# Kernel tuning notes

Measured on AMD Instinct MI355X. Metric: run time of the kernel, lower is better.

Reference implementation:

```python
import jax, jax.numpy as jnp
import numpy as np

D_MODEL = 1024
NUM_HEADS = 4
EXPAND_K = 1.0
EXPAND_V = 2.0
KEY_DIM = int(D_MODEL * EXPAND_K)      # 1024
VALUE_DIM = int(D_MODEL * EXPAND_V)    # 2048
HEAD_K = KEY_DIM // NUM_HEADS          # 256
HEAD_V = VALUE_DIM // NUM_HEADS        # 512
CHUNK = 64
EPS = 1e-5
ROPE_BASE = 10000.0


def setup_inputs() -> dict:
    key = jax.random.key(0)
    ks = jax.random.split(key, 7)
    B, T = 4, 2048
    s = 0.02
    return {
        "x": jax.random.normal(ks[0], (B, T, D_MODEL), dtype=jnp.float32),
        "Wq": jax.random.normal(ks[1], (KEY_DIM, D_MODEL), dtype=jnp.float32) * s,
        "Wk": jax.random.normal(ks[2], (KEY_DIM, D_MODEL), dtype=jnp.float32) * s,
        "Wv": jax.random.normal(ks[3], (VALUE_DIM, D_MODEL), dtype=jnp.float32) * s,
        "Wg": jax.random.normal(ks[4], (VALUE_DIM, D_MODEL), dtype=jnp.float32) * s,
        "Wo": jax.random.normal(ks[5], (D_MODEL, VALUE_DIM), dtype=jnp.float32) * s,
        "gnorm_w": jnp.ones((HEAD_V,), dtype=jnp.float32),
    }


def _apply_rotary(q, k):
    # q,k: [B,T,H,dk]; NeoX-style (non-interleaved) rotary on full head dim
    d = q.shape[-1]
    half = d // 2
    inv_freq = 1.0 / (ROPE_BASE ** (jnp.arange(0, d, 2, dtype=jnp.float32) / d))
    t = jnp.arange(q.shape[1], dtype=jnp.float32)
    freqs = t[:, None] * inv_freq[None, :]          # [T, d/2]
    cos = jnp.cos(freqs)[None, :, None, :]
    sin = jnp.sin(freqs)[None, :, None, :]

    def rot(x):
        x1, x2 = x[..., :half], x[..., half:]
        return jnp.concatenate([x1 * cos - x2 * sin, x2 * cos + x1 * sin], axis=-1)

    return rot(q), rot(k)


def _chunk_retention(q, k, v, gamma):
    # q,k: [B,T,H,dk]; v: [B,T,H,dv]; gamma: [H] per-head decay
    B, T, H, dk = q.shape
    dv = v.shape[-1]
    C = CHUNK
    N = T // C
    qc = q.reshape(B, N, C, H, dk).transpose(1, 0, 3, 2, 4)  # [N,B,H,C,dk]
    kc = k.reshape(B, N, C, H, dk).transpose(1, 0, 3, 2, 4)
    vc = v.reshape(B, N, C, H, dv).transpose(1, 0, 3, 2, 4)  # [N,B,H,C,dv]

    i = jnp.arange(C, dtype=jnp.float32)
    cross_dec = gamma[:, None] ** (i + 1.0)          # [H,C] gamma^{i+1}: query decay vs incoming state
    k_dec = gamma[:, None] ** (C - 1.0 - i)          # [H,C] key decay toward chunk end
    diff = i[:, None] - i[None, :]                   # [C,C]
    mask = jnp.where(diff >= 0, gamma[:, None, None] ** diff, 0.0)  # [H,C,C]
    gC = gamma ** C                                  # [H]

    def step(S, inp):
        # S: [B,H,dk,dv]
        qb, kb, vb = inp
        attn = jnp.einsum('bhid,bhjd->bhij', qb, kb) * mask
        o_intra = jnp.einsum('bhij,bhjv->bhiv', attn, vb)
        o_inter = jnp.einsum('bhid,bhdv->bhiv', qb * cross_dec[:, :, None], S)
        S_new = gC[:, None, None] * S + jnp.einsum('bhjd,bhjv->bhdv', kb * k_dec[:, :, None], vb)
        return S_new, o_intra + o_inter

    S0 = jnp.zeros((B, H, dk, dv), dtype=q.dtype)
    _, o = jax.lax.scan(step, S0, (qc, kc, vc))      # o: [N,B,H,C,dv]
    return o.transpose(1, 0, 3, 2, 4).reshape(B, T, H, dv)


def reference(x, Wq, Wk, Wv, Wg, Wo, gnorm_w):
    B, T, _ = x.shape
    H = NUM_HEADS
    q = (x @ Wq.T).reshape(B, T, H, HEAD_K)
    k = (x @ Wk.T).reshape(B, T, H, HEAD_K)
    v = (x @ Wv.T).reshape(B, T, H, HEAD_V)
    g = (x @ Wg.T).reshape(B, T, H, HEAD_V)

    q, k = _apply_rotary(q, k)
    q = q * (HEAD_K ** -0.5)

    # fixed multi-scale decays: gamma_h = 1 - 2^{-5-h}
    gamma = 1.0 - jnp.exp2(-5.0 - jnp.arange(H, dtype=jnp.float32))

    o = _chunk_retention(q, k, v, gamma)             # [B,T,H,dv]

    # per-head RMSNorm + swish gate, then output projection
    var = jnp.mean(o * o, axis=-1, keepdims=True)
    o = o * jax.lax.rsqrt(var + EPS) * gnorm_w
    o = o * (g * jax.nn.sigmoid(g))
    return o.reshape(B, T, H * HEAD_V) @ Wo.T
```

## Files before the change

kernel.cpp:

```cpp
#include <hip/hip_runtime.h>
#include <cstdint>
#include <cstddef>

#define T_SEQ 2048
#define DM    1024
#define HK    256
#define HV    512
#define NH    4
#define KDIM  1024
#define VDIM  2048

typedef __attribute__((ext_vector_type(8))) short bf16x8;
typedef __attribute__((ext_vector_type(4))) float f32x4;
#define AS1 __attribute__((address_space(1)))
#define AS3 __attribute__((address_space(3)))

static __device__ inline unsigned short f2bf(float f) {
  unsigned u = __float_as_uint(f);
  unsigned rnd = 0x7fffu + ((u >> 16) & 1u);
  return (unsigned short)((u + rnd) >> 16);
}
static __device__ inline float bf2f(unsigned short h) {
  unsigned u = ((unsigned)h) << 16;
  return __uint_as_float(u);
}

__global__ __launch_bounds__(256) void cast_all(const float* __restrict__ x,
                                                const float* __restrict__ Wq,
                                                const float* __restrict__ Wk,
                                                const float* __restrict__ Wv,
                                                const float* __restrict__ Wg,
                                                const float* __restrict__ Wo,
                                                unsigned short* __restrict__ xh,  unsigned short* __restrict__ xl,
                                                unsigned short* __restrict__ wqh, unsigned short* __restrict__ wql,
                                                unsigned short* __restrict__ wkh, unsigned short* __restrict__ wkl,
                                                unsigned short* __restrict__ wvh, unsigned short* __restrict__ wvl,
                                                unsigned short* __restrict__ wgh, unsigned short* __restrict__ wgl,
                                                unsigned short* __restrict__ woh, unsigned short* __restrict__ wol) {
  const int bx = blockIdx.x;
  const float* in; unsigned short* hi; unsigned short* lo; int rel;
  if (bx < 8192)       { in = x;  hi = xh;  lo = xl;  rel = bx; }
  else if (bx < 9216)  { in = Wq; hi = wqh; lo = wql; rel = bx - 8192; }
  else if (bx < 10240) { in = Wk; hi = wkh; lo = wkl; rel = bx - 9216; }
  else if (bx < 12288) { in = Wv; hi = wvh; lo = wvl; rel = bx - 10240; }
  else if (bx < 14336) { in = Wg; hi = wgh; lo = wgl; rel = bx - 12288; }
  else                 { in = Wo; hi = woh; lo = wol; rel = bx - 14336; }
  int i = rel * 256 + threadIdx.x;
  float4 v = ((const float4*)in)[i];
  ushort4 h, l;
  h.x = f2bf(v.x); l.x = f2bf(v.x - bf2f(h.x));
  h.y = f2bf(v.y); l.y = f2bf(v.y - bf2f(h.y));
  h.z = f2bf(v.z); l.z = f2bf(v.z - bf2f(h.z));
  h.w = f2bf(v.w); l.w = f2bf(v.w - bf2f(h.w));
  ((ushort4*)hi)[i] = h;
  ((ushort4*)lo)[i] = l;
}

__global__ __launch_bounds__(256) void gemm_bf16s(const unsigned short* __restrict__ Ah,
                                                  const unsigned short* __restrict__ Al,
                                                  const unsigned short* __restrict__ Wh,
                                                  const unsigned short* __restrict__ Wl,
                                                  float* __restrict__ C,
                                                  int M, int N, int K) {
  __shared__ unsigned short AhS[128 * 32];
  __shared__ unsigned short AlS[128 * 32];
  __shared__ unsigned short WhS[128 * 32];
  __shared__ unsigned short WlS[128 * 32];
  const int t = threadIdx.x;
  const int l = t & 63;
  const int w = t >> 6;
  const int bm = blockIdx.y * 128;
  const int bn = blockIdx.x * 128;
  const int wm = (w >> 1) * 64;
  const int wn = (w & 1) * 64;

  f32x4 acc[4][4];
#pragma unroll
  for (int i = 0; i < 4; ++i)
#pragma unroll
    for (int j = 0; j < 4; ++j)
#pragma unroll
      for (int r = 0; r < 4; ++r) acc[i][j][r] = 0.f;

  const int srow = w * 32 + (l >> 2);
  const int scol = (l & 3) * 8;
  const size_t gOffA = (size_t)(bm + srow) * K + scol;
  const size_t gOffW = (size_t)(bn + srow) * K + scol;
  const size_t rowStep = (size_t)16 * K;
  unsigned short* lAh0 = &AhS[(w * 32) * 32];
  unsigned short* lAh1 = &AhS[(w * 32 + 16) * 32];
  unsigned short* lAl0 = &AlS[(w * 32) * 32];
  unsigned short* lAl1 = &AlS[(w * 32 + 16) * 32];
  unsigned short* lWh0 = &WhS[(w * 32) * 32];
  unsigned short* lWh1 = &WhS[(w * 32 + 16) * 32];
  unsigned short* lWl0 = &WlS[(w * 32) * 32];
  unsigned short* lWl1 = &WlS[(w * 32 + 16) * 32];

  for (int k0 = 0; k0 < K; k0 += 32) {
    __syncthreads();
    __builtin_amdgcn_global_load_lds((const AS1 void*)(Ah + gOffA + k0),           (AS3 void*)lAh0, 16, 0, 0);
    __builtin_amdgcn_global_load_lds((const AS1 void*)(Ah + gOffA + rowStep + k0), (AS3 void*)lAh1, 16, 0, 0);
    __builtin_amdgcn_global_load_lds((const AS1 void*)(Al + gOffA + k0),           (AS3 void*)lAl0, 16, 0, 0);
    __builtin_amdgcn_global_load_lds((const AS1 void*)(Al + gOffA + rowStep + k0), (AS3 void*)lAl1, 16, 0, 0);
    __builtin_amdgcn_global_load_lds((const AS1 void*)(Wh + gOffW + k0),           (AS3 void*)lWh0, 16, 0, 0);
    __builtin_amdgcn_global_load_lds((const AS1 void*)(Wh + gOffW + rowStep + k0), (AS3 void*)lWh1, 16, 0, 0);
    __builtin_amdgcn_global_load_lds((const AS1 void*)(Wl + gOffW + k0),           (AS3 void*)lWl0, 16, 0, 0);
    __builtin_amdgcn_global_load_lds((const AS1 void*)(Wl + gOffW + rowStep + k0), (AS3 void*)lWl1, 16, 0, 0);
    __syncthreads();

    bf16x8 ah[4], al[4], bh[4], bl[4];
#pragma unroll
    for (int i = 0; i < 4; ++i) {
      int aoff = (wm + i * 16 + (l & 15)) * 32 + (l >> 4) * 8;
      int boff = (wn + i * 16 + (l & 15)) * 32 + (l >> 4) * 8;
      ah[i] = *(const bf16x8*)&AhS[aoff];
      al[i] = *(const bf16x8*)&AlS[aoff];
      bh[i] = *(const bf16x8*)&WhS[boff];
      bl[i] = *(const bf16x8*)&WlS[boff];
    }
#pragma unroll
    for (int i = 0; i < 4; ++i)
#pragma unroll
      for (int j = 0; j < 4; ++j) {
        acc[i][j] = __builtin_amdgcn_mfma_f32_16x16x32_bf16(ah[i], bh[j], acc[i][j], 0, 0, 0);
        acc[i][j] = __builtin_amdgcn_mfma_f32_16x16x32_bf16(ah[i], bl[j], acc[i][j], 0, 0, 0);
        acc[i][j] = __builtin_amdgcn_mfma_f32_16x16x32_bf16(al[i], bh[j], acc[i][j], 0, 0, 0);
      }
  }

  const int cr = (l >> 4) * 4;
  const int cc = l & 15;
#pragma unroll
  for (int i = 0; i < 4; ++i)
#pragma unroll
    for (int j = 0; j < 4; ++j)
#pragma unroll
      for (int r = 0; r < 4; ++r)
        C[(size_t)(bm + wm + i * 16 + cr + r) * N + (bn + wn + j * 16 + cc)] = acc[i][j][r];
}

__global__ __launch_bounds__(256) void gemm_qkv(const unsigned short* __restrict__ Ah,
                                                const unsigned short* __restrict__ Al,
                                                const unsigned short* __restrict__ wqh,
                                                const unsigned short* __restrict__ wql,
                                                const unsigned short* __restrict__ wkh,
                                                const unsigned short* __restrict__ wkl,
                                                const unsigned short* __restrict__ wvh,
                                                const unsigned short* __restrict__ wvl,
                                                float* __restrict__ q,
                                                float* __restrict__ kk,
                                                float* __restrict__ v) {
  const int K = 1024;
  const int bx = blockIdx.x;
  const unsigned short* Wh; const unsigned short* Wl; float* C; int N; int bn;
  if (bx < 8)       { Wh = wqh; Wl = wql; C = q;  N = 1024; bn = bx * 128; }
  else if (bx < 16) { Wh = wkh; Wl = wkl; C = kk; N = 1024; bn = (bx - 8) * 128; }
  else              { Wh = wvh; Wl = wvl; C = v;  N = 2048; bn = (bx - 16) * 128; }

  __shared__ unsigned short AhS[128 * 32];
  __shared__ unsigned short AlS[128 * 32];
  __shared__ unsigned short WhS[128 * 32];
  __shared__ unsigned short WlS[128 * 32];
  const int t = threadIdx.x;
  const int l = t & 63;
  const int w = t >> 6;
  const int bm = blockIdx.y * 128;
  const int wm = (w >> 1) * 64;
  const int wn = (w & 1) * 64;

  f32x4 acc[4][4];
#pragma unroll
  for (int i = 0; i < 4; ++i)
#pragma unroll
    for (int j = 0; j < 4; ++j)
#pragma unroll
      for (int r = 0; r < 4; ++r) acc[i][j][r] = 0.f;

  const int srow = w * 32 + (l >> 2);
  const int scol = (l & 3) * 8;
  const size_t gOffA = (size_t)(bm + srow) * K + scol;
  const size_t gOffW = (size_t)(bn + srow) * K + scol;
  const size_t rowStep = (size_t)16 * K;
  unsigned short* lAh0 = &AhS[(w * 32) * 32];
  unsigned short* lAh1 = &AhS[(w * 32 + 16) * 32];
  unsigned short* lAl0 = &AlS[(w * 32) * 32];
  unsigned short* lAl1 = &AlS[(w * 32 + 16) * 32];
  unsigned short* lWh0 = &WhS[(w * 32) * 32];
  unsigned short* lWh1 = &WhS[(w * 32 + 16) * 32];
  unsigned short* lWl0 = &WlS[(w * 32) * 32];
  unsigned short* lWl1 = &WlS[(w * 32 + 16) * 32];

  for (int k0 = 0; k0 < K; k0 += 32) {
    __syncthreads();
    __builtin_amdgcn_global_load_lds((const AS1 void*)(Ah + gOffA + k0),           (AS3 void*)lAh0, 16, 0, 0);
    __builtin_amdgcn_global_load_lds((const AS1 void*)(Ah + gOffA + rowStep + k0), (AS3 void*)lAh1, 16, 0, 0);
    __builtin_amdgcn_global_load_lds((const AS1 void*)(Al + gOffA + k0),           (AS3 void*)lAl0, 16, 0, 0);
    __builtin_amdgcn_global_load_lds((const AS1 void*)(Al + gOffA + rowStep + k0), (AS3 void*)lAl1, 16, 0, 0);
    __builtin_amdgcn_global_load_lds((const AS1 void*)(Wh + gOffW + k0),           (AS3 void*)lWh0, 16, 0, 0);
    __builtin_amdgcn_global_load_lds((const AS1 void*)(Wh + gOffW + rowStep + k0), (AS3 void*)lWh1, 16, 0, 0);
    __builtin_amdgcn_global_load_lds((const AS1 void*)(Wl + gOffW + k0),           (AS3 void*)lWl0, 16, 0, 0);
    __builtin_amdgcn_global_load_lds((const AS1 void*)(Wl + gOffW + rowStep + k0), (AS3 void*)lWl1, 16, 0, 0);
    __syncthreads();

    bf16x8 ah[4], al[4], bh[4], bl[4];
#pragma unroll
    for (int i = 0; i < 4; ++i) {
      int aoff = (wm + i * 16 + (l & 15)) * 32 + (l >> 4) * 8;
      int boff = (wn + i * 16 + (l & 15)) * 32 + (l >> 4) * 8;
      ah[i] = *(const bf16x8*)&AhS[aoff];
      al[i] = *(const bf16x8*)&AlS[aoff];
      bh[i] = *(const bf16x8*)&WhS[boff];
      bl[i] = *(const bf16x8*)&WlS[boff];
    }
#pragma unroll
    for (int i = 0; i < 4; ++i)
#pragma unroll
      for (int j = 0; j < 4; ++j) {
        acc[i][j] = __builtin_amdgcn_mfma_f32_16x16x32_bf16(ah[i], bh[j], acc[i][j], 0, 0, 0);
        acc[i][j] = __builtin_amdgcn_mfma_f32_16x16x32_bf16(ah[i], bl[j], acc[i][j], 0, 0, 0);
        acc[i][j] = __builtin_amdgcn_mfma_f32_16x16x32_bf16(al[i], bh[j], acc[i][j], 0, 0, 0);
      }
  }

  const int cr = (l >> 4) * 4;
  const int cc = l & 15;
#pragma unroll
  for (int i = 0; i < 4; ++i)
#pragma unroll
    for (int j = 0; j < 4; ++j)
#pragma unroll
      for (int r = 0; r < 4; ++r)
        C[(size_t)(bm + wm + i * 16 + cr + r) * N + (bn + wn + j * 16 + cc)] = acc[i][j][r];
}

__global__ __launch_bounds__(256) void rope_kernel(float* __restrict__ q,
                                                   float* __restrict__ k) {
  int idx = blockIdx.x * 256 + threadIdx.x;
  int f  = idx & 127;
  int h  = (idx >> 7) & 3;
  int tt = (idx >> 9) & 2047;
  int b  = idx >> 20;
  size_t a0 = ((size_t)(b * T_SEQ + tt)) * KDIM + h * HK + f;
  size_t a1 = a0 + 128;
  float invf = powf(10000.0f, -(float)f * (1.0f / 128.0f));
  float ang  = (float)tt * invf;
  float s, c;
  sincosf(ang, &s, &c);
  float q1 = q[a0], q2 = q[a1];
  q[a0] = (q1 * c - q2 * s) * 0.0625f;
  q[a1] = (q2 * c + q1 * s) * 0.0625f;
  float k1 = k[a0], k2 = k[a1];
  k[a0] = k1 * c - k2 * s;
  k[a1] = k2 * c + k1 * s;
}

__global__ __launch_bounds__(256) void retn_intra(const float* __restrict__ q,
                                                  const float* __restrict__ k,
                                                  const float* __restrict__ v,
                                                  float* __restrict__ o) {
  const int n = blockIdx.x, h = blockIdx.y, b = blockIdx.z;
  const int t = threadIdx.x;
  const int t0 = n * 64;
  __shared__ float gpow[65];
  __shared__ __align__(16) float qS[64][68];
  __shared__ __align__(16) float kS[64][68];
  __shared__ __align__(16) float attnS[64][68];
  if (t <= 64) {
    float gamma = 1.0f - exp2f(-5.0f - (float)h);
    gpow[t] = powf(gamma, (float)t);
  }
  const size_t baseQK = (size_t)(b * T_SEQ + t0) * KDIM + h * HK;
  const size_t baseV  = (size_t)(b * T_SEQ + t0) * VDIM + h * HV;
  const int i0 = (t >> 4) * 4;
  const int j0 = (t & 15) * 4;
  float acc[4][4] = {};
  for (int s = 0; s < 4; ++s) {
    __syncthreads();
    __builtin_amdgcn_sched_barrier(0);
#pragma unroll
    for (int r = 0; r < 4; ++r) {
      int idx = t + 256 * r;
      int row = idx >> 4, c4 = (idx & 15) * 4;
      *(float4*)&qS[row][c4] = *(const float4*)&q[baseQK + (size_t)row * KDIM + s * 64 + c4];
      *(float4*)&kS[row][c4] = *(const float4*)&k[baseQK + (size_t)row * KDIM + s * 64 + c4];
    }
    __syncthreads();
    __builtin_amdgcn_sched_barrier(0);
    for (int d = 0; d < 64; d += 4) {
      float4 a0 = *(const float4*)&qS[i0 + 0][d];
      float4 a1 = *(const float4*)&qS[i0 + 1][d];
      float4 a2 = *(const float4*)&qS[i0 + 2][d];
      float4 a3 = *(const float4*)&qS[i0 + 3][d];
      float4 b0 = *(const float4*)&kS[j0 + 0][d];
      float4 b1 = *(const float4*)&kS[j0 + 1][d];
      float4 b2 = *(const float4*)&kS[j0 + 2][d];
      float4 b3 = *(const float4*)&kS[j0 + 3][d];
      acc[0][0]=fmaf(a0.x,b0.x,acc[0][0]); acc[0][0]=fmaf(a0.y,b0.y,acc[0][0]); acc[0][0]=fmaf(a0.z,b0.z,acc[0][0]); acc[0][0]=fmaf(a0.w,b0.w,acc[0][0]);
      acc[0][1]=fmaf(a0.x,b1.x,acc[0][1]); acc[0][1]=fmaf(a0.y,b1.y,acc[0][1]); acc[0][1]=fmaf(a0.z,b1.z,acc[0][1]); acc[0][1]=fmaf(a0.w,b1.w,acc[0][1]);
      acc[0][2]=fmaf(a0.x,b2.x,acc[0][2]); acc[0][2]=fmaf(a0.y,b2.y,acc[0][2]); acc[0][2]=fmaf(a0.z,b2.z,acc[0][2]); acc[0][2]=fmaf(a0.w,b2.w,acc[0][2]);
      acc[0][3]=fmaf(a0.x,b3.x,acc[0][3]); acc[0][3]=fmaf(a0.y,b3.y,acc[0][3]); acc[0][3]=fmaf(a0.z,b3.z,acc[0][3]); acc[0][3]=fmaf(a0.w,b3.w,acc[0][3]);
      acc[1][0]=fmaf(a1.x,b0.x,acc[1][0]); acc[1][0]=fmaf(a1.y,b0.y,acc[1][0]); acc[1][0]=fmaf(a1.z,b0.z,acc[1][0]); acc[1][0]=fmaf(a1.w,b0.w,acc[1][0]);
      acc[1][1]=fmaf(a1.x,b1.x,acc[1][1]); acc[1][1]=fmaf(a1.y,b1.y,acc[1][1]); acc[1][1]=fmaf(a1.z,b1.z,acc[1][1]); acc[1][1]=fmaf(a1.w,b1.w,acc[1][1]);
      acc[1][2]=fmaf(a1.x,b2.x,acc[1][2]); acc[1][2]=fmaf(a1.y,b2.y,acc[1][2]); acc[1][2]=fmaf(a1.z,b2.z,acc[1][2]); acc[1][2]=fmaf(a1.w,b2.w,acc[1][2]);
      acc[1][3]=fmaf(a1.x,b3.x,acc[1][3]); acc[1][3]=fmaf(a1.y,b3.y,acc[1][3]); acc[1][3]=fmaf(a1.z,b3.z,acc[1][3]); acc[1][3]=fmaf(a1.w,b3.w,acc[1][3]);
      acc[2][0]=fmaf(a2.x,b0.x,acc[2][0]); acc[2][0]=fmaf(a2.y,b0.y,acc[2][0]); acc[2][0]=fmaf(a2.z,b0.z,acc[2][0]); acc[2][0]=fmaf(a2.w,b0.w,acc[2][0]);
      acc[2][1]=fmaf(a2.x,b1.x,acc[2][1]); acc[2][1]=fmaf(a2.y,b1.y,acc[2][1]); acc[2][1]=fmaf(a2.z,b1.z,acc[2][1]); acc[2][1]=fmaf(a2.w,b1.w,acc[2][1]);
      acc[2][2]=fmaf(a2.x,b2.x,acc[2][2]); acc[2][2]=fmaf(a2.y,b2.y,acc[2][2]); acc[2][2]=fmaf(a2.z,b2.z,acc[2][2]); acc[2][2]=fmaf(a2.w,b2.w,acc[2][2]);
      acc[2][3]=fmaf(a2.x,b3.x,acc[2][3]); acc[2][3]=fmaf(a2.y,b3.y,acc[2][3]); acc[2][3]=fmaf(a2.z,b3.z,acc[2][3]); acc[2][3]=fmaf(a2.w,b3.w,acc[2][3]);
      acc[3][0]=fmaf(a3.x,b0.x,acc[3][0]); acc[3][0]=fmaf(a3.y,b0.y,acc[3][0]); acc[3][0]=fmaf(a3.z,b0.z,acc[3][0]); acc[3][0]=fmaf(a3.w,b0.w,acc[3][0]);
      acc[3][1]=fmaf(a3.x,b1.x,acc[3][1]); acc[3][1]=fmaf(a3.y,b1.y,acc[3][1]); acc[3][1]=fmaf(a3.z,b1.z,acc[3][1]); acc[3][1]=fmaf(a3.w,b1.w,acc[3][1]);
      acc[3][2]=fmaf(a3.x,b2.x,acc[3][2]); acc[3][2]=fmaf(a3.y,b2.y,acc[3][2]); acc[3][2]=fmaf(a3.z,b2.z,acc[3][2]); acc[3][2]=fmaf(a3.w,b2.w,acc[3][2]);
      acc[3][3]=fmaf(a3.x,b3.x,acc[3][3]); acc[3][3]=fmaf(a3.y,b3.y,acc[3][3]); acc[3][3]=fmaf(a3.z,b3.z,acc[3][3]); acc[3][3]=fmaf(a3.w,b3.w,acc[3][3]);
    }
  }
  __syncthreads();
#pragma unroll
  for (int ii = 0; ii < 4; ++ii)
#pragma unroll
    for (int jj = 0; jj < 4; ++jj) {
      int i = i0 + ii, j = j0 + jj;
      attnS[i][j] = (i >= j) ? acc[ii][jj] * gpow[i - j] : 0.0f;
    }
  float (*vS)[68] = qS;
  for (int vb = 0; vb < 8; ++vb) {
    __syncthreads();
    __builtin_amdgcn_sched_barrier(0);
#pragma unroll
    for (int r = 0; r < 4; ++r) {
      int idx = t + 256 * r;
      int row = idx >> 4, c4 = (idx & 15) * 4;
      *(float4*)&vS[row][c4] = *(const float4*)&v[baseV + (size_t)row * VDIM + vb * 64 + c4];
    }
    __syncthreads();
    __builtin_amdgcn_sched_barrier(0);
    float oa[4][4] = {};
    for (int j = 0; j < 64; j += 4) {
      float4 p0 = *(const float4*)&attnS[i0 + 0][j];
      float4 p1 = *(const float4*)&attnS[i0 + 1][j];
      float4 p2 = *(const float4*)&attnS[i0 + 2][j];
      float4 p3 = *(const float4*)&attnS[i0 + 3][j];
      float4 v0 = *(const float4*)&vS[j + 0][j0];
      float4 v1 = *(const float4*)&vS[j + 1][j0];
      float4 v2 = *(const float4*)&vS[j + 2][j0];
      float4 v3 = *(const float4*)&vS[j + 3][j0];
      oa[0][0]=fmaf(p0.x,v0.x,oa[0][0]); oa[0][0]=fmaf(p0.y,v1.x,oa[0][0]); oa[0][0]=fmaf(p0.z,v2.x,oa[0][0]); oa[0][0]=fmaf(p0.w,v3.x,oa[0][0]);
      oa[0][1]=fmaf(p0.x,v0.y,oa[0][1]); oa[0][1]=fmaf(p0.y,v1.y,oa[0][1]); oa[0][1]=fmaf(p0.z,v2.y,oa[0][1]); oa[0][1]=fmaf(p0.w,v3.y,oa[0][1]);
      oa[0][2]=fmaf(p0.x,v0.z,oa[0][2]); oa[0][2]=fmaf(p0.y,v1.z,oa[0][2]); oa[0][2]=fmaf(p0.z,v2.z,oa[0][2]); oa[0][2]=fmaf(p0.w,v3.z,oa[0][2]);
      oa[0][3]=fmaf(p0.x,v0.w,oa[0][3]); oa[0][3]=fmaf(p0.y,v1.w,oa[0][3]); oa[0][3]=fmaf(p0.z,v2.w,oa[0][3]); oa[0][3]=fmaf(p0.w,v3.w,oa[0][3]);
      oa[1][0]=fmaf(p1.x,v0.x,oa[1][0]); oa[1][0]=fmaf(p1.y,v1.x,oa[1][0]); oa[1][0]=fmaf(p1.z,v2.x,oa[1][0]); oa[1][0]=fmaf(p1.w,v3.x,oa[1][0]);
      oa[1][1]=fmaf(p1.x,v0.y,oa[1][1]); oa[1][1]=fmaf(p1.y,v1.y,oa[1][1]); oa[1][1]=fmaf(p1.z,v2.y,oa[1][1]); oa[1][1]=fmaf(p1.w,v3.y,oa[1][1]);
      oa[1][2]=fmaf(p1.x,v0.z,oa[1][2]); oa[1][2]=fmaf(p1.y,v1.z,oa[1][2]); oa[1][2]=fmaf(p1.z,v2.z,oa[1][2]); oa[1][2]=fmaf(p1.w,v3.z,oa[1][2]);
      oa[1][3]=fmaf(p1.x,v0.w,oa[1][3]); oa[1][3]=fmaf(p1.y,v1.w,oa[1][3]); oa[1][3]=fmaf(p1.z,v2.w,oa[1][3]); oa[1][3]=fmaf(p1.w,v3.w,oa[1][3]);
      oa[2][0]=fmaf(p2.x,v0.x,oa[2][0]); oa[2][0]=fmaf(p2.y,v1.x,oa[2][0]); oa[2][0]=fmaf(p2.z,v2.x,oa[2][0]); oa[2][0]=fmaf(p2.w,v3.x,oa[2][0]);
      oa[2][1]=fmaf(p2.x,v0.y,oa[2][1]); oa[2][1]=fmaf(p2.y,v1.y,oa[2][1]); oa[2][1]=fmaf(p2.z,v2.y,oa[2][1]); oa[2][1]=fmaf(p2.w,v3.y,oa[2][1]);
      oa[2][2]=fmaf(p2.x,v0.z,oa[2][2]); oa[2][2]=fmaf(p2.y,v1.z,oa[2][2]); oa[2][2]=fmaf(p2.z,v2.z,oa[2][2]); oa[2][2]=fmaf(p2.w,v3.z,oa[2][2]);
      oa[2][3]=fmaf(p2.x,v0.w,oa[2][3]); oa[2][3]=fmaf(p2.y,v1.w,oa[2][3]); oa[2][3]=fmaf(p2.z,v2.w,oa[2][3]); oa[2][3]=fmaf(p2.w,v3.w,oa[2][3]);
      oa[3][0]=fmaf(p3.x,v0.x,oa[3][0]); oa[3][0]=fmaf(p3.y,v1.x,oa[3][0]); oa[3][0]=fmaf(p3.z,v2.x,oa[3][0]); oa[3][0]=fmaf(p3.w,v3.x,oa[3][0]);
      oa[3][1]=fmaf(p3.x,v0.y,oa[3][1]); oa[3][1]=fmaf(p3.y,v1.y,oa[3][1]); oa[3][1]=fmaf(p3.z,v2.y,oa[3][1]); oa[3][1]=fmaf(p3.w,v3.y,oa[3][1]);
      oa[3][2]=fmaf(p3.x,v0.z,oa[3][2]); oa[3][2]=fmaf(p3.y,v1.z,oa[3][2]); oa[3][2]=fmaf(p3.z,v2.z,oa[3][2]); oa[3][2]=fmaf(p3.w,v3.z,oa[3][2]);
      oa[3][3]=fmaf(p3.x,v0.w,oa[3][3]); oa[3][3]=fmaf(p3.y,v1.w,oa[3][3]); oa[3][3]=fmaf(p3.z,v2.w,oa[3][3]); oa[3][3]=fmaf(p3.w,v3.w,oa[3][3]);
    }
#pragma unroll
    for (int ii = 0; ii < 4; ++ii)
      *(float4*)&o[baseV + (size_t)(i0 + ii) * VDIM + vb * 64 + j0] =
          make_float4(oa[ii][0], oa[ii][1], oa[ii][2], oa[ii][3]);
  }
}


__global__ __launch_bounds__(256) void retn_gstate(const float* __restrict__ k,
                                                   const float* __restrict__ v,
                                                   float* __restrict__ Tbuf) {
  const int bh = blockIdx.x; const int b = bh >> 2, h = bh & 3;
  const int g = blockIdx.y;
  const int dkt = blockIdx.z >> 2, dvt = blockIdx.z & 3;
  const int t = threadIdx.x;
  __shared__ float gpow[65];
  __shared__ __align__(16) float kS[64][132];
  __shared__ __align__(16) float vS[64][132];
  if (t <= 64) gpow[t] = powf(1.0f - exp2f(-5.0f - (float)h), (float)t);
  __syncthreads();
  const float gC = gpow[64];
  const size_t baseK = (size_t)(b * T_SEQ + g * 512) * KDIM + h * HK + dkt * 128;
  const size_t baseV = (size_t)(b * T_SEQ + g * 512) * VDIM + h * HV + dvt * 128;
  const int dk0 = (t & 15) * 4;
  const int c0  = (t >> 4) * 4;
  float S[2][2][4][4] = {};
  for (int c = 0; c < 8; ++c) {
    const int t0 = c * 64;
    __syncthreads();
    __builtin_amdgcn_sched_barrier(0);
#pragma unroll
    for (int r = 0; r < 8; ++r) {
      int idx = t + 256 * r; int row = idx >> 5, c4 = (idx & 31) * 4;
      float4 kv = *(const float4*)&k[baseK + (size_t)(t0 + row) * KDIM + c4];
      float kd = gpow[63 - row];
      kv.x *= kd; kv.y *= kd; kv.z *= kd; kv.w *= kd;
      *(float4*)&kS[row][c4] = kv;
      *(float4*)&vS[row][c4] = *(const float4*)&v[baseV + (size_t)(t0 + row) * VDIM + c4];
    }
    __syncthreads();
    __builtin_amdgcn_sched_barrier(0);
#pragma unroll
    for (int p = 0; p < 2; ++p)
#pragma unroll
      for (int qh = 0; qh < 2; ++qh)
#pragma unroll
        for (int ii = 0; ii < 4; ++ii)
#pragma unroll
          for (int jj = 0; jj < 4; ++jj) S[p][qh][ii][jj] *= gC;
    for (int j = 0; j < 64; ++j) {
      float4 ka = *(const float4*)&kS[j][dk0];
      float4 kb = *(const float4*)&kS[j][dk0 + 64];
      float4 va = *(const float4*)&vS[j][c0];
      float4 vb = *(const float4*)&vS[j][c0 + 64];
      float kr[8] = {ka.x, ka.y, ka.z, ka.w, kb.x, kb.y, kb.z, kb.w};
      float vr[8] = {va.x, va.y, va.z, va.w, vb.x, vb.y, vb.z, vb.w};
#pragma unroll
      for (int ii = 0; ii < 8; ++ii)
#pragma unroll
        for (int jj = 0; jj < 8; ++jj)
          S[ii >> 2][jj >> 2][ii & 3][jj & 3] =
              fmaf(kr[ii], vr[jj], S[ii >> 2][jj >> 2][ii & 3][jj & 3]);
    }
  }
  const size_t tbRow = ((size_t)g * 16 + bh) * 256 + dkt * 128 + dk0;
  const size_t tbCol = (size_t)dvt * 128 + c0;
#pragma unroll
  for (int p = 0; p < 2; ++p)
#pragma unroll
    for (int ii = 0; ii < 4; ++ii) {
      size_t rowb = (tbRow + p * 64 + ii) * 512 + tbCol;
      *(float4*)&Tbuf[rowb]      = make_float4(S[p][0][ii][0], S[p][0][ii][1], S[p][0][ii][2], S[p][0][ii][3]);
      *(float4*)&Tbuf[rowb + 64] = make_float4(S[p][1][ii][0], S[p][1][ii][1], S[p][1][ii][2], S[p][1][ii][3]);
    }
}

__global__ __launch_bounds__(256) void retn_scan(float* __restrict__ Tbuf) {
  int i = blockIdx.x * 256 + threadIdx.x;
  int h = (i >> 15) & 3;
  float gamma = 1.0f - exp2f(-5.0f - (float)h);
  float gG = powf(gamma, 512.0f);
  float4* T = (float4*)Tbuf;
  const int slab = 524288;
  float4 t0 = T[i], t1 = T[i + slab], t2 = T[i + 2 * slab];
  float4 s2, s3;
  s2.x = fmaf(gG, t0.x, t1.x); s2.y = fmaf(gG, t0.y, t1.y);
  s2.z = fmaf(gG, t0.z, t1.z); s2.w = fmaf(gG, t0.w, t1.w);
  s3.x = fmaf(gG, s2.x, t2.x); s3.y = fmaf(gG, s2.y, t2.y);
  s3.z = fmaf(gG, s2.z, t2.z); s3.w = fmaf(gG, s2.w, t2.w);
  T[i + slab] = s2; T[i + 2 * slab] = s3;
}

__global__ __launch_bounds__(256) void retn_inter2(const float* __restrict__ q,
                                                   const float* __restrict__ k,
                                                   const float* __restrict__ v,
                                                   float* __restrict__ o,
                                                   const float* __restrict__ Sbuf) {
  const int bh = blockIdx.x; const int b = bh >> 2, h = bh & 3;
  const int g = blockIdx.y;
  const int dvt = blockIdx.z;
  const int t = threadIdx.x;
  __shared__ float gpow[65];
  __shared__ __align__(16) float qS[64][68];
  __shared__ __align__(16) float kS[64][68];
  __shared__ __align__(16) float sS[64][68];
  __shared__ __align__(16) float vS[64][68];
  if (t <= 64) gpow[t] = powf(1.0f - exp2f(-5.0f - (float)h), (float)t);
  __syncthreads();
  const float gC = gpow[64];
  const int rq = (t & 15) * 4;
  const int c0 = (t >> 4) * 4;
  const int i0 = (t >> 4) * 4;
  const int v0 = (t & 15) * 4;
  const size_t baseQK = (size_t)(b * T_SEQ + g * 512) * KDIM + h * HK;
  const size_t baseV  = (size_t)(b * T_SEQ + g * 512) * VDIM + h * HV + (size_t)dvt * 64;

  float S[4][4][4];
  if (g > 0) {
    const size_t sb = (((size_t)(g - 1) * 16 + bh) * 256) * 512 + (size_t)dvt * 64 + c0;
#pragma unroll
    for (int b4 = 0; b4 < 4; ++b4)
#pragma unroll
      for (int i = 0; i < 4; ++i) {
        float4 tmp = *(const float4*)&Sbuf[sb + (size_t)(b4 * 64 + rq + i) * 512];
        S[b4][i][0] = tmp.x; S[b4][i][1] = tmp.y; S[b4][i][2] = tmp.z; S[b4][i][3] = tmp.w;
      }
  } else {
#pragma unroll
    for (int b4 = 0; b4 < 4; ++b4)
#pragma unroll
      for (int i = 0; i < 4; ++i) {
        S[b4][i][0] = 0.f; S[b4][i][1] = 0.f; S[b4][i][2] = 0.f; S[b4][i][3] = 0.f;
      }
  }

  for (int c = 0; c < 8; ++c) {
    const int t0 = c * 64;
    const bool doO = (g > 0 || c > 0);
    __syncthreads();
    __builtin_amdgcn_sched_barrier(0);
#pragma unroll
    for (int r = 0; r < 4; ++r) {
      int idx = t + 256 * r; int row = idx >> 4, c4 = (idx & 15) * 4;
      *(float4*)&vS[row][c4] = *(const float4*)&v[baseV + (size_t)(t0 + row) * VDIM + c4];
    }
    float oa[4][4] = {};
#pragma unroll
    for (int b4 = 0; b4 < 4; ++b4) {
      __syncthreads();
      __builtin_amdgcn_sched_barrier(0);
      if (doO) {
#pragma unroll
        for (int i = 0; i < 4; ++i)
          *(float4*)&sS[rq + i][c0] =
              make_float4(S[b4][i][0], S[b4][i][1], S[b4][i][2], S[b4][i][3]);
#pragma unroll
        for (int r = 0; r < 4; ++r) {
          int idx = t + 256 * r; int row = idx >> 4, c4 = (idx & 15) * 4;
          float4 qv = *(const float4*)&q[baseQK + (size_t)(t0 + row) * KDIM + b4 * 64 + c4];
          float gp = gpow[row + 1];
          qv.x *= gp; qv.y *= gp; qv.z *= gp; qv.w *= gp;
          *(float4*)&qS[row][c4] = qv;
        }
      }
#pragma unroll
      for (int r = 0; r < 4; ++r) {
        int idx = t + 256 * r; int row = idx >> 4, c4 = (idx & 15) * 4;
        float4 kv = *(const float4*)&k[baseQK + (size_t)(t0 + row) * KDIM + b4 * 64 + c4];
        float kd = gpow[63 - row];
        kv.x *= kd; kv.y *= kd; kv.z *= kd; kv.w *= kd;
        *(float4*)&kS[row][c4] = kv;
      }
      __syncthreads();
      __builtin_amdgcn_sched_barrier(0);
      if (doO) {
        for (int d = 0; d < 64; d += 4) {
          float4 a0 = *(const float4*)&qS[i0 + 0][d];
          float4 a1 = *(const float4*)&qS[i0 + 1][d];
          float4 a2 = *(const float4*)&qS[i0 + 2][d];
          float4 a3 = *(const float4*)&qS[i0 + 3][d];
          float4 s0 = *(const float4*)&sS[d + 0][v0];
          float4 s1 = *(const float4*)&sS[d + 1][v0];
          float4 s2 = *(const float4*)&sS[d + 2][v0];
          float4 s3 = *(const float4*)&sS[d + 3][v0];
          oa[0][0]=fmaf(a0.x,s0.x,oa[0][0]); oa[0][0]=fmaf(a0.y,s1.x,oa[0][0]); oa[0][0]=fmaf(a0.z,s2.x,oa[0][0]); oa[0][0]=fmaf(a0.w,s3.x,oa[0][0]);
          oa[0][1]=fmaf(a0.x,s0.y,oa[0][1]); oa[0][1]=fmaf(a0.y,s1.y,oa[0][1]); oa[0][1]=fmaf(a0.z,s2.y,oa[0][1]); oa[0][1]=fmaf(a0.w,s3.y,oa[0][1]);
          oa[0][2]=fmaf(a0.x,s0.z,oa[0][2]); oa[0][2]=fmaf(a0.y,s1.z,oa[0][2]); oa[0][2]=fmaf(a0.z,s2.z,oa[0][2]); oa[0][2]=fmaf(a0.w,s3.z,oa[0][2]);
          oa[0][3]=fmaf(a0.x,s0.w,oa[0][3]); oa[0][3]=fmaf(a0.y,s1.w,oa[0][3]); oa[0][3]=fmaf(a0.z,s2.w,oa[0][3]); oa[0][3]=fmaf(a0.w,s3.w,oa[0][3]);
          oa[1][0]=fmaf(a1.x,s0.x,oa[1][0]); oa[1][0]=fmaf(a1.y,s1.x,oa[1][0]); oa[1][0]=fmaf(a1.z,s2.x,oa[1][0]); oa[1][0]=fmaf(a1.w,s3.x,oa[1][0]);
          oa[1][1]=fmaf(a1.x,s0.y,oa[1][1]); oa[1][1]=fmaf(a1.y,s1.y,oa[1][1]); oa[1][1]=fmaf(a1.z,s2.y,oa[1][1]); oa[1][1]=fmaf(a1.w,s3.y,oa[1][1]);
          oa[1][2]=fmaf(a1.x,s0.z,oa[1][2]); oa[1][2]=fmaf(a1.y,s1.z,oa[1][2]); oa[1][2]=fmaf(a1.z,s2.z,oa[1][2]); oa[1][2]=fmaf(a1.w,s3.z,oa[1][2]);
          oa[1][3]=fmaf(a1.x,s0.w,oa[1][3]); oa[1][3]=fmaf(a1.y,s1.w,oa[1][3]); oa[1][3]=fmaf(a1.z,s2.w,oa[1][3]); oa[1][3]=fmaf(a1.w,s3.w,oa[1][3]);
          oa[2][0]=fmaf(a2.x,s0.x,oa[2][0]); oa[2][0]=fmaf(a2.y,s1.x,oa[2][0]); oa[2][0]=fmaf(a2.z,s2.x,oa[2][0]); oa[2][0]=fmaf(a2.w,s3.x,oa[2][0]);
          oa[2][1]=fmaf(a2.x,s0.y,oa[2][1]); oa[2][1]=fmaf(a2.y,s1.y,oa[2][1]); oa[2][1]=fmaf(a2.z,s2.y,oa[2][1]); oa[2][1]=fmaf(a2.w,s3.y,oa[2][1]);
          oa[2][2]=fmaf(a2.x,s0.z,oa[2][2]); oa[2][2]=fmaf(a2.y,s1.z,oa[2][2]); oa[2][2]=fmaf(a2.z,s2.z,oa[2][2]); oa[2][2]=fmaf(a2.w,s3.z,oa[2][2]);
          oa[2][3]=fmaf(a2.x,s0.w,oa[2][3]); oa[2][3]=fmaf(a2.y,s1.w,oa[2][3]); oa[2][3]=fmaf(a2.z,s2.w,oa[2][3]); oa[2][3]=fmaf(a2.w,s3.w,oa[2][3]);
          oa[3][0]=fmaf(a3.x,s0.x,oa[3][0]); oa[3][0]=fmaf(a3.y,s1.x,oa[3][0]); oa[3][0]=fmaf(a3.z,s2.x,oa[3][0]); oa[3][0]=fmaf(a3.w,s3.x,oa[3][0]);
          oa[3][1]=fmaf(a3.x,s0.y,oa[3][1]); oa[3][1]=fmaf(a3.y,s1.y,oa[3][1]); oa[3][1]=fmaf(a3.z,s2.y,oa[3][1]); oa[3][1]=fmaf(a3.w,s3.y,oa[3][1]);
          oa[3][2]=fmaf(a3.x,s0.z,oa[3][2]); oa[3][2]=fmaf(a3.y,s1.z,oa[3][2]); oa[3][2]=fmaf(a3.z,s2.z,oa[3][2]); oa[3][2]=fmaf(a3.w,s3.z,oa[3][2]);
          oa[3][3]=fmaf(a3.x,s0.w,oa[3][3]); oa[3][3]=fmaf(a3.y,s1.w,oa[3][3]); oa[3][3]=fmaf(a3.z,s2.w,oa[3][3]); oa[3][3]=fmaf(a3.w,s3.w,oa[3][3]);
        }
      }
#pragma unroll
      for (int ii = 0; ii < 4; ++ii) {
        S[b4][ii][0] *= gC; S[b4][ii][1] *= gC; S[b4][ii][2] *= gC; S[b4][ii][3] *= gC;
      }
      for (int j = 0; j < 64; ++j) {
        float4 kv = *(const float4*)&kS[j][rq];
        float4 vv = *(const float4*)&vS[j][c0];
        S[b4][0][0] = fmaf(kv.x, vv.x, S[b4][0][0]); S[b4][0][1] = fmaf(kv.x, vv.y, S[b4][0][1]);
        S[b4][0][2] = fmaf(kv.x, vv.z, S[b4][0][2]); S[b4][0][3] = fmaf(kv.x, vv.w, S[b4][0][3]);
        S[b4][1][0] = fmaf(kv.y, vv.x, S[b4][1][0]); S[b4][1][1] = fmaf(kv.y, vv.y, S[b4][1][1]);
        S[b4][1][2] = fmaf(kv.y, vv.z, S[b4][1][2]); S[b4][1][3] = fmaf(kv.y, vv.w, S[b4][1][3]);
        S[b4][2][0] = fmaf(kv.z, vv.x, S[b4][2][0]); S[b4][2][1] = fmaf(kv.z, vv.y, S[b4][2][1]);
        S[b4][2][2] = fmaf(kv.z, vv.z, S[b4][2][2]); S[b4][2][3] = fmaf(kv.z, vv.w, S[b4][2][3]);
        S[b4][3][0] = fmaf(kv.w, vv.x, S[b4][3][0]); S[b4][3][1] = fmaf(kv.w, vv.y, S[b4][3][1]);
        S[b4][3][2] = fmaf(kv.w, vv.z, S[b4][3][2]); S[b4][3][3] = fmaf(kv.w, vv.w, S[b4][3][3]);
      }
    }
    if (doO) {
#pragma unroll
      for (int ii = 0; ii < 4; ++ii) {
        size_t addr = baseV + (size_t)(t0 + i0 + ii) * VDIM + v0;
        float4 ov = *(const float4*)&o[addr];
        ov.x += oa[ii][0]; ov.y += oa[ii][1]; ov.z += oa[ii][2]; ov.w += oa[ii][3];
        *(float4*)&o[addr] = ov;
      }
    }
  }
}

__global__ __launch_bounds__(256) void norm_gate_cast(const float* __restrict__ o,
                                                      const float* __restrict__ g,
                                                      const float* __restrict__ gnw,
                                                      unsigned short* __restrict__ oh,
                                                      unsigned short* __restrict__ ol) {
  const int row = blockIdx.x;
  const size_t base = (size_t)row * 512;
  const int t = threadIdx.x;
  float x0 = o[base + t], x1 = o[base + t + 256];
  float ss = x0 * x0 + x1 * x1;
#pragma unroll
  for (int off = 32; off > 0; off >>= 1) ss += __shfl_down(ss, off, 64);
  __shared__ float wsum[4];
  if ((t & 63) == 0) wsum[t >> 6] = ss;
  __syncthreads();
  float tot = wsum[0] + wsum[1] + wsum[2] + wsum[3];
  float scale = rsqrtf(tot * (1.0f / 512.0f) + 1e-5f);
  float g0 = g[base + t], g1 = g[base + t + 256];
  float r0 = x0 * scale * gnw[t]       * (g0 / (1.0f + expf(-g0)));
  float r1 = x1 * scale * gnw[t + 256] * (g1 / (1.0f + expf(-g1)));
  unsigned short h0 = f2bf(r0);
  unsigned short h1 = f2bf(r1);
  oh[base + t]       = h0; ol[base + t]       = f2bf(r0 - bf2f(h0));
  oh[base + t + 256] = h1; ol[base + t + 256] = f2bf(r1 - bf2f(h1));
}

extern "C" void kernel_launch(void* const* d_in, const int* in_sizes, int n_in,
                              void* d_out, int out_size, void* d_ws, size_t ws_size,
                              hipStream_t stream) {
  const float* x   = (const float*)d_in[0];
  const float* Wq  = (const float*)d_in[1];
  const float* Wk  = (const float*)d_in[2];
  const float* Wv  = (const float*)d_in[3];
  const float* Wg  = (const float*)d_in[4];
  const float* Wo  = (const float*)d_in[5];
  const float* gnw = (const float*)d_in[6];
  float* out = (float*)d_out;

  const size_t M8 = (size_t)8192;
  float* q  = (float*)d_ws;
  float* kk = q  + M8 * 1024;
  float* v  = kk + M8 * 1024;
  float* o  = v  + M8 * 2048;
  unsigned short* xh  = (unsigned short*)(o + M8 * 2048);
  unsigned short* xl  = xh  + M8 * 1024;
  unsigned short* wqh = xl  + M8 * 1024;
  unsigned short* wql = wqh + (size_t)1024 * 1024;
  unsigned short* wkh = wql + (size_t)1024 * 1024;
  unsigned short* wkl = wkh + (size_t)1024 * 1024;
  unsigned short* wvh = wkl + (size_t)1024 * 1024;
  unsigned short* wvl = wvh + (size_t)2048 * 1024;
  unsigned short* wgh = wvl + (size_t)2048 * 1024;
  unsigned short* wgl = wgh + (size_t)2048 * 1024;
  unsigned short* woh = wgl + (size_t)2048 * 1024;
  unsigned short* wol = woh + (size_t)2048 * 1024;
  unsigned short* oh  = (unsigned short*)v;
  unsigned short* ol  = oh + M8 * 2048;
  float* g = q;
  float* Tbuf = (float*)d_out;

  dim3 blk(256);
  cast_all<<<dim3(16384), blk, 0, stream>>>(x, Wq, Wk, Wv, Wg, Wo,
                                            xh, xl, wqh, wql, wkh, wkl,
                                            wvh, wvl, wgh, wgl, woh, wol);

  gemm_qkv<<<dim3(32, 64), blk, 0, stream>>>(xh, xl, wqh, wql, wkh, wkl, wvh, wvl, q, kk, v);
  rope_kernel<<<dim3(16384), blk, 0, stream>>>(q, kk);
  retn_gstate<<<dim3(16, 3, 8), blk, 0, stream>>>(kk, v, Tbuf);
  retn_scan<<<dim3(2048), blk, 0, stream>>>(Tbuf);
  retn_intra<<<dim3(32, 4, 4),  blk, 0, stream>>>(q, kk, v, o);
  retn_inter2<<<dim3(16, 4, 8), blk, 0, stream>>>(q, kk, v, o, Tbuf);
  gemm_bf16s<<<dim3(16, 64), blk, 0, stream>>>(xh, xl, wgh, wgl, g, 8192, 2048, 1024);
  norm_gate_cast<<<dim3(32768), blk, 0, stream>>>(o, g, gnw, oh, ol);
  gemm_bf16s<<<dim3(8, 64),  blk, 0, stream>>>(oh, ol, woh, wol, out, 8192, 1024, 2048);
}
```

Measured before the change: 1.017 ms.

## Precompute RoPE table, prefetch q/k tiles in inter kernel, raise MFMA-loop priority

Adds a small kernel that precomputes the cos/sin table once, so the rope kernel no longer evaluates powf and sincosf per element. In the inter-chunk retention kernel, the next q/k sub-tile is loaded into registers while the current one is processed, which hides global load latency behind compute. It also raises wave priority around the inner FMA loops with s_setprio. The costs are extra register pressure from the prefetch buffers and a table stored in a spare region of the output buffer.

```diff
diff --git a/kernel.cpp b/kernel.cpp
--- a/kernel.cpp
+++ b/kernel.cpp
@@ -233,8 +233,20 @@
         C[(size_t)(bm + wm + i * 16 + cr + r) * N + (bn + wn + j * 16 + cc)] = acc[i][j][r];
 }
 
+__global__ __launch_bounds__(256) void rope_tab(float2* __restrict__ tab) {
+  int i = blockIdx.x * 256 + threadIdx.x;
+  int f  = i & 127;
+  int tt = i >> 7;
+  float invf = powf(10000.0f, -(float)f * (1.0f / 128.0f));
+  float ang  = (float)tt * invf;
+  float s, c;
+  sincosf(ang, &s, &c);
+  tab[i] = make_float2(c, s);
+}
+
 __global__ __launch_bounds__(256) void rope_kernel(float* __restrict__ q,
-                                                   float* __restrict__ k) {
+                                                   float* __restrict__ k,
+                                                   const float2* __restrict__ tab) {
   int idx = blockIdx.x * 256 + threadIdx.x;
   int f  = idx & 127;
   int h  = (idx >> 7) & 3;
@@ -242,10 +254,8 @@
   int b  = idx >> 20;
   size_t a0 = ((size_t)(b * T_SEQ + tt)) * KDIM + h * HK + f;
   size_t a1 = a0 + 128;
-  float invf = powf(10000.0f, -(float)f * (1.0f / 128.0f));
-  float ang  = (float)tt * invf;
-  float s, c;
-  sincosf(ang, &s, &c);
+  float2 cs = tab[tt * 128 + f];
+  float c = cs.x, s = cs.y;
   float q1 = q[a0], q2 = q[a1];
   q[a0] = (q1 * c - q2 * s) * 0.0625f;
   q[a1] = (q2 * c + q1 * s) * 0.0625f;
@@ -401,6 +411,7 @@
     }
     __syncthreads();
     __builtin_amdgcn_sched_barrier(0);
+    __builtin_amdgcn_s_setprio(1);
 #pragma unroll
     for (int p = 0; p < 2; ++p)
 #pragma unroll
@@ -423,6 +434,7 @@
           S[ii >> 2][jj >> 2][ii & 3][jj & 3] =
               fmaf(kr[ii], vr[jj], S[ii >> 2][jj >> 2][ii & 3][jj & 3]);
     }
+    __builtin_amdgcn_s_setprio(0);
   }
   const size_t tbRow = ((size_t)g * 16 + bh) * 256 + dkt * 128 + dk0;
   const size_t tbCol = (size_t)dvt * 128 + c0;
@@ -475,6 +487,8 @@
   const int v0 = (t & 15) * 4;
   const size_t baseQK = (size_t)(b * T_SEQ + g * 512) * KDIM + h * HK;
   const size_t baseV  = (size_t)(b * T_SEQ + g * 512) * VDIM + h * HV + (size_t)dvt * 64;
+  const int srow0 = t >> 4;
+  const int scol  = (t & 15) * 4;
 
   float S[4][4][4];
   if (g > 0) {
@@ -495,6 +509,8 @@
       }
   }
 
+  float4 pq[4], pk[4];
+
   for (int c = 0; c < 8; ++c) {
     const int t0 = c * 64;
     const bool doO = (g > 0 || c > 0);
@@ -502,8 +518,14 @@
     __builtin_amdgcn_sched_barrier(0);
 #pragma unroll
     for (int r = 0; r < 4; ++r) {
-      int idx = t + 256 * r; int row = idx >> 4, c4 = (idx & 15) * 4;
-      *(float4*)&vS[row][c4] = *(const float4*)&v[baseV + (size_t)(t0 + row) * VDIM + c4];
+      int row = srow0 + 16 * r;
+      *(float4*)&vS[row][scol] = *(const float4*)&v[baseV + (size_t)(t0 + row) * VDIM + scol];
+    }
+#pragma unroll
+    for (int r = 0; r < 4; ++r) {
+      int row = srow0 + 16 * r;
+      pq[r] = *(const float4*)&q[baseQK + (size_t)(t0 + row) * KDIM + 0 * 64 + scol];
+      pk[r] = *(const float4*)&k[baseQK + (size_t)(t0 + row) * KDIM + 0 * 64 + scol];
     }
     float oa[4][4] = {};
 #pragma unroll
@@ -517,23 +539,32 @@
               make_float4(S[b4][i][0], S[b4][i][1], S[b4][i][2], S[b4][i][3]);
 #pragma unroll
         for (int r = 0; r < 4; ++r) {
-          int idx = t + 256 * r; int row = idx >> 4, c4 = (idx & 15) * 4;
-          float4 qv = *(const float4*)&q[baseQK + (size_t)(t0 + row) * KDIM + b4 * 64 + c4];
+          int row = srow0 + 16 * r;
           float gp = gpow[row + 1];
+          float4 qv = pq[r];
           qv.x *= gp; qv.y *= gp; qv.z *= gp; qv.w *= gp;
-          *(float4*)&qS[row][c4] = qv;
+          *(float4*)&qS[row][scol] = qv;
         }
       }
 #pragma unroll
       for (int r = 0; r < 4; ++r) {
-        int idx = t + 256 * r; int row = idx >> 4, c4 = (idx & 15) * 4;
-        float4 kv = *(const float4*)&k[baseQK + (size_t)(t0 + row) * KDIM + b4 * 64 + c4];
+        int row = srow0 + 16 * r;
         float kd = gpow[63 - row];
+        float4 kv = pk[r];
         kv.x *= kd; kv.y *= kd; kv.z *= kd; kv.w *= kd;
-        *(float4*)&kS[row][c4] = kv;
+        *(float4*)&kS[row][scol] = kv;
+      }
+      if (b4 < 3) {
+#pragma unroll
+        for (int r = 0; r < 4; ++r) {
+          int row = srow0 + 16 * r;
+          pq[r] = *(const float4*)&q[baseQK + (size_t)(t0 + row) * KDIM + (b4 + 1) * 64 + scol];
+          pk[r] = *(const float4*)&k[baseQK + (size_t)(t0 + row) * KDIM + (b4 + 1) * 64 + scol];
+        }
       }
       __syncthreads();
       __builtin_amdgcn_sched_barrier(0);
+      __builtin_amdgcn_s_setprio(1);
       if (doO) {
         for (int d = 0; d < 64; d += 4) {
           float4 a0 = *(const float4*)&qS[i0 + 0][d];
@@ -578,6 +609,7 @@
         S[b4][3][0] = fmaf(kv.w, vv.x, S[b4][3][0]); S[b4][3][1] = fmaf(kv.w, vv.y, S[b4][3][1]);
         S[b4][3][2] = fmaf(kv.w, vv.z, S[b4][3][2]); S[b4][3][3] = fmaf(kv.w, vv.w, S[b4][3][3]);
       }
+      __builtin_amdgcn_s_setprio(0);
     }
     if (doO) {
 #pragma unroll
@@ -650,14 +682,16 @@
   unsigned short* ol  = oh + M8 * 2048;
   float* g = q;
   float* Tbuf = (float*)d_out;
+  float2* rtab = (float2*)((float*)d_out + 6291456);
 
   dim3 blk(256);
+  rope_tab<<<dim3(1024), blk, 0, stream>>>(rtab);
   cast_all<<<dim3(16384), blk, 0, stream>>>(x, Wq, Wk, Wv, Wg, Wo,
                                             xh, xl, wqh, wql, wkh, wkl,
                                             wvh, wvl, wgh, wgl, woh, wol);
 
   gemm_qkv<<<dim3(32, 64), blk, 0, stream>>>(xh, xl, wqh, wql, wkh, wkl, wvh, wvl, q, kk, v);
-  rope_kernel<<<dim3(16384), blk, 0, stream>>>(q, kk);
+  rope_kernel<<<dim3(16384), blk, 0, stream>>>(q, kk, rtab);
   retn_gstate<<<dim3(16, 3, 8), blk, 0, stream>>>(kk, v, Tbuf);
   retn_scan<<<dim3(2048), blk, 0, stream>>>(Tbuf);
   retn_intra<<<dim3(32, 4, 4),  blk, 0, stream>>>(q, kk, v, o);
```

After: 969.4 us. 1.05x faster.
